# Optimization experiments

Hardware: AMD Instinct MI355X
Metric: run time of the kernel (lower is better)

The kernel has to match this reference:

```python
import jax, jax.numpy as jnp
import numpy as np

B, D, F, E, G = 2048, 1024, 4096, 16, 2
EPS = 1e-9
LN_EPS = 1e-5


def setup_inputs() -> dict:
    key = jax.random.key(0)
    ks = jax.random.split(key, 10)
    s_in = 1.0 / np.sqrt(D)
    s_out = 1.0 / np.sqrt(F)
    return {
        "cycle_curve_data": jax.random.normal(ks[0], (B, D), jnp.float32),
        "logits": jax.random.normal(ks[1], (B, E), jnp.float32),
        "moe_masks": jax.random.randint(ks[2], (B, E), 0, 2, jnp.int32),
        "ew_in": jax.random.uniform(ks[3], (E, D, F), jnp.float32, -s_in, s_in),
        "ew_out": jax.random.uniform(ks[4], (E, F, D), jnp.float32, -s_out, s_out),
        "eb_out": jax.random.uniform(ks[5], (E, D), jnp.float32, -s_out, s_out),
        "gw_in": jax.random.uniform(ks[6], (G, D, F), jnp.float32, -s_in, s_in),
        "gw_out": jax.random.uniform(ks[7], (G, F, D), jnp.float32, -s_out, s_out),
        "gb_out": jax.random.uniform(ks[8], (G, D), jnp.float32, -s_out, s_out),
        "ln_gamma": jnp.ones((D,), jnp.float32),
        "ln_beta": jnp.zeros((D,), jnp.float32),
    }


def _moe_forward(x, logits, moe_masks, ew_in, ew_out, eb_out, gw_in, gw_out, gb_out, ln_gamma, ln_beta):
    b = x.shape[0]
    mask = (moe_masks == 1).astype(logits.dtype)          # [B,E]
    raw = jax.nn.softmax(logits, axis=1)                   # [B,E]
    gates = raw * mask
    gates = gates / (jnp.sum(gates, axis=1, keepdims=True) + EPS)
    # Per-expert MLPBlockGELU over all tokens; gate=0 zeroes out non-dispatched
    # tokens exactly as MOEDispatcher.combine does.
    h = jax.nn.gelu(jnp.einsum('bd,edf->ebf', x, ew_in), approximate=False)  # [E,B,F]
    eout = jnp.einsum('ebf,efd->ebd', h, ew_out) + eb_out[:, None, :]        # [E,B,D]
    moe_out = jnp.einsum('be,ebd->bd', gates, eout).astype(jnp.bfloat16)     # combine + bf16 cast
    # general experts (dense, added to routed output; bf16+f32 promotes to f32)
    gh = jax.nn.gelu(jnp.einsum('bd,gdf->gbf', x, gw_in), approximate=False)
    gout = jnp.einsum('gbf,gfd->gbd', gh, gw_out) + gb_out[:, None, :]       # [G,B,D]
    final = jnp.sum(gout, axis=0) + moe_out                                  # f32
    # residual + LayerNorm
    y = final + x
    mu = jnp.mean(y, axis=-1, keepdims=True)
    var = jnp.mean(jnp.square(y - mu), axis=-1, keepdims=True)
    final_out = (y - mu) * jax.lax.rsqrt(var + LN_EPS) * ln_gamma + ln_beta
    # training losses
    expert_logits = jnp.mean(raw, axis=0)                                    # [E]
    expert_sample_count = jnp.sum((gates != 0).astype(raw.dtype), axis=0) / b
    aug_loss = jnp.mean(expert_logits * expert_sample_count)
    s = jnp.sum(raw * mask) / b
    guide_loss = (1.0 - s) * (1.0 - s)
    return final_out, aug_loss, guide_loss


def reference(cycle_curve_data, logits, moe_masks, ew_in, ew_out, eb_out, gw_in, gw_out, gb_out, ln_gamma, ln_beta):
    return _moe_forward(cycle_curve_data, logits, moe_masks, ew_in, ew_out, eb_out,
                        gw_in, gw_out, gb_out, ln_gamma, ln_beta)
```

## Files before the change

### kernel.cpp

```cpp
#include <hip/hip_runtime.h>
#include <hip/hip_bf16.h>

#define B_TOK 2048
#define DDIM 1024
#define FDIM 4096
#define NE 16
#define NG 2
#define BD ((long)B_TOK * DDIM)

typedef unsigned short u16;
typedef __attribute__((ext_vector_type(8))) short bf16x8;
typedef __attribute__((ext_vector_type(4))) float f32x4;

__device__ inline u16 f2bf(float x) {
  union { float f; unsigned u; } v; v.f = x;
  return (u16)((v.u + 0x7fffu + ((v.u >> 16) & 1u)) >> 16);
}
__device__ inline float bfround(float x) {
  union { float f; unsigned u; } v; v.f = x;
  v.u = ((v.u + 0x7fffu + ((v.u >> 16) & 1u)) >> 16) << 16;
  return v.f;
}
__device__ inline float fast_erf(float x) {
  float ax = fabsf(x);
  float t = __builtin_amdgcn_rcpf(1.0f + 0.3275911f * ax);
  float poly = t * (0.254829592f + t * (-0.284496736f + t * (1.421413741f +
               t * (-1.453152027f + t * 1.061405429f))));
  float r = 1.0f - poly * __expf(-ax * ax);
  return copysignf(r, x);
}
__device__ inline float gelu_exact(float x) {
  return 0.5f * x * (1.0f + fast_erf(x * 0.70710678118654752440f));
}
__device__ inline void gload16(const void* g, void* l) {
  __builtin_amdgcn_global_load_lds((const __attribute__((address_space(1))) void*)g,
                                   (__attribute__((address_space(3))) void*)l, 16, 0, 0);
}
__device__ inline float waveSum(float v) {
  v += __shfl_down(v, 32); v += __shfl_down(v, 16); v += __shfl_down(v, 8);
  v += __shfl_down(v, 4);  v += __shfl_down(v, 2);  v += __shfl_down(v, 1);
  return v;
}

__global__ __launch_bounds__(256) void gating_kernel(
    const float* __restrict__ logits, const int* __restrict__ masks,
    float* __restrict__ gates, float* __restrict__ loss)
{
  const int b = blockIdx.x * 256 + threadIdx.x;
  const int lane = threadIdx.x & 63;
  const float* lr = logits + (long)b * NE;
  const int*   mr = masks  + (long)b * NE;
  float raw[NE]; int mk[NE];
  float mx = -1e30f;
#pragma unroll
  for (int e = 0; e < NE; ++e) { raw[e] = lr[e]; mx = fmaxf(mx, raw[e]); }
  float s = 0.f;
#pragma unroll
  for (int e = 0; e < NE; ++e) { raw[e] = expf(raw[e] - mx); s += raw[e]; }
  float inv = 1.0f / s;
#pragma unroll
  for (int e = 0; e < NE; ++e) raw[e] *= inv;
  float gs = 0.f;
#pragma unroll
  for (int e = 0; e < NE; ++e) { mk[e] = (mr[e] == 1); gs += mk[e] ? raw[e] : 0.f; }
  float ginv = 1.0f / (gs + 1e-9f);
  float* gr = gates + (long)b * NE;
#pragma unroll
  for (int e = 0; e < NE; ++e) gr[e] = (mk[e] ? raw[e] : 0.f) * ginv;
#pragma unroll
  for (int e = 0; e < NE; ++e) {
    float cs = waveSum(raw[e]);
    float cc = waveSum(mk[e] ? 1.f : 0.f);
    if (lane == 0) { atomicAdd(&loss[e], cs); atomicAdd(&loss[NE + e], cc); }
  }
  float t = waveSum(gs);
  if (lane == 0) atomicAdd(&loss[32], t);
}

__global__ void finalize_loss(const float* __restrict__ loss, float* __restrict__ out2) {
  if (threadIdx.x == 0) {
    float aug = 0.f;
    for (int e = 0; e < NE; ++e)
      aug += (loss[e] / (float)B_TOK) * (loss[NE + e] / (float)B_TOK);
    aug *= (1.0f / NE);
    float s = loss[32] / (float)B_TOK;
    out2[0] = aug;
    out2[1] = (1.f - s) * (1.f - s);
  }
}

__global__ __launch_bounds__(256) void compact_kernel(
    const int* __restrict__ masks, int* __restrict__ tok,
    int* __restrict__ pos, int* __restrict__ cnts)
{
  const int e = blockIdx.x, tid = threadIdx.x;
  const int lane = tid & 63, wave = tid >> 6;
  __shared__ int wcnt[4];
  __shared__ int runbase;
  if (tid == 0) runbase = 0;
  __syncthreads();
  for (int b0 = 0; b0 < B_TOK; b0 += 256) {
    int b = b0 + tid;
    int m = (masks[(long)b * NE + e] == 1);
    unsigned long long bal = __ballot(m);
    int pre = __popcll(bal & ((1ull << lane) - 1ull));
    if (lane == 0) wcnt[wave] = __popcll(bal);
    __syncthreads();
    int base = runbase;
    for (int w = 0; w < wave; ++w) base += wcnt[w];
    if (m) {
      int p = base + pre;
      tok[(e << 11) + p] = b;
      pos[(long)b * NE + e] = p;
    } else {
      pos[(long)b * NE + e] = -1;
    }
    __syncthreads();
    if (tid == 0) runbase += wcnt[0] + wcnt[1] + wcnt[2] + wcnt[3];
    __syncthreads();
  }
  const int cnt = runbase;
  const int cnt_pad = (cnt + 127) & ~127;
  for (int i = cnt + tid; i < cnt_pad; i += 256)
    tok[(e << 11) + i] = 0;
  if (tid == 0) { cnts[e] = cnt; cnts[NE + e] = cnt_pad; }
}

__global__ __launch_bounds__(256) void cvt_x_kernel(const float* __restrict__ x, u16* __restrict__ xb) {
  long i = ((long)blockIdx.x * 256 + threadIdx.x) * 4;
  float4 v = *(const float4*)&x[i];
  ushort4 o; o.x = f2bf(v.x); o.y = f2bf(v.y); o.z = f2bf(v.z); o.w = f2bf(v.w);
  *(ushort4*)&xb[i] = o;
}

__global__ __launch_bounds__(256) void bias_init_kernel(
    const float* __restrict__ gates, const float* __restrict__ eb,
    float* __restrict__ moe_bias)
{
  long i = (long)blockIdx.x * 256 + threadIdx.x;
  int b = (int)(i >> 10), d = (int)(i & 1023);
  const float* gr = gates + (long)b * NE;
  float s = 0.f;
#pragma unroll
  for (int e = 0; e < NE; ++e) s += gr[e] * eb[e * DDIM + d];
  moe_bias[i] = s;
}

__global__ __launch_bounds__(256) void transpose_cvt(
    const float* __restrict__ src, u16* __restrict__ dst,
    int R, int C, long sZ, long dZ)
{
  __shared__ float t[64][65];
  const float* s = src + (long)blockIdx.z * sZ;
  u16* d = dst + (long)blockIdx.z * dZ;
  const int c0 = blockIdx.x * 64, r0 = blockIdx.y * 64;
  const int tid = threadIdx.x;
#pragma unroll
  for (int it = 0; it < 4; ++it) {
    int idx = tid + it * 256;
    int r = idx >> 4, cq = (idx & 15) * 4;
    float4 v = *(const float4*)&s[(long)(r0 + r) * C + c0 + cq];
    t[r][cq] = v.x; t[r][cq + 1] = v.y; t[r][cq + 2] = v.z; t[r][cq + 3] = v.w;
  }
  __syncthreads();
#pragma unroll
  for (int it = 0; it < 4; ++it) {
    int idx = tid + it * 256;
    int c = idx >> 4, rq = (idx & 15) * 4;
    ushort4 o;
    o.x = f2bf(t[rq][c]); o.y = f2bf(t[rq+1][c]); o.z = f2bf(t[rq+2][c]); o.w = f2bf(t[rq+3][c]);
    *(ushort4*)&d[(long)(c0 + c) * R + r0 + rq] = o;
  }
}

template<int MODE>
__global__ __launch_bounds__(256) void gemm128(
    const u16* __restrict__ A, int lda, long aZ,
    const u16* __restrict__ Bm, int ldb, long bZ,
    int klen,
    u16* __restrict__ H, long hZ,
    float* __restrict__ C, long cZ,
    const int* __restrict__ tok, const int* __restrict__ cnts, int ebase)
{
  int lin = ((int)blockIdx.z * gridDim.y + blockIdx.y) * gridDim.x + blockIdx.x;
  const int T = gridDim.x * gridDim.y * gridDim.z;
  lin = (lin & 7) * (T >> 3) + (lin >> 3);
  const int bx = lin % gridDim.x;
  const int rest = lin / gridDim.x;
  const int by = rest % gridDim.y;
  const int bz = rest / gridDim.y;

  const int zi = (MODE == 2) ? (bz >> 2) : bz;
  const int ks = (MODE == 2) ? (bz & 3) * klen : 0;
  const int m0 = by * 128, n0 = bx * 128;
  if (MODE != 2 && cnts && m0 >= cnts[NE + ebase + zi]) return;

  __shared__ u16 sA[3][128 * 32];
  __shared__ u16 sB[3][128 * 32];
  const u16* Az = A + (long)zi * aZ;
  const u16* Bz = Bm + (long)zi * bZ;
  const int tid = threadIdx.x, lane = tid & 63, wave = tid >> 6;

  const int off = tid * 16;
  const int sr  = off >> 6;
  const int ske = (off & 63) >> 1;
  int arow0 = m0 + sr, arow1 = m0 + sr + 64;
  if (MODE == 0 && tok) {
    const int* tz = tok + ((ebase + zi) << 11);
    arow0 = tz[arow0]; arow1 = tz[arow1];
  }
  const u16* gA0 = Az + (long)arow0 * lda + ks + ske;
  const u16* gA1 = Az + (long)arow1 * lda + ks + ske;
  const u16* gB0 = Bz + (long)(n0 + sr) * ldb + ks + ske;
  const u16* gB1 = gB0 + (long)64 * ldb;

  const int wr = wave >> 1, wc = wave & 1;
  const int fr = lane & 15, fk = (lane >> 4) * 8;
  const int rAo = (wr * 64 + fr) * 32 + fk;
  const int rBo = (wc * 64 + fr) * 32 + fk;

  f32x4 zero = {0.f, 0.f, 0.f, 0.f};
  f32x4 acc[4][4];
#pragma unroll
  for (int m = 0; m < 4; ++m)
#pragma unroll
    for (int n = 0; n < 4; ++n) acc[m][n] = zero;

  auto STAGE = [&](u16* dA, u16* dB, int t) {
    const int kk = t << 5;
    gload16(gA0 + kk, dA + wave * 512);
    gload16(gA1 + kk, dA + 2048 + wave * 512);
    gload16(gB0 + kk, dB + wave * 512);
    gload16(gB1 + kk, dB + 2048 + wave * 512);
  };
  auto COMPUTE = [&](const u16* bA, const u16* bB) {
    bf16x8 av[4], bv[4];
#pragma unroll
    for (int m = 0; m < 4; ++m) av[m] = *(const bf16x8*)(bA + rAo + m * 512);
#pragma unroll
    for (int n = 0; n < 4; ++n) bv[n] = *(const bf16x8*)(bB + rBo + n * 512);
#pragma unroll
    for (int m = 0; m < 4; ++m)
#pragma unroll
      for (int n = 0; n < 4; ++n)
        acc[m][n] = __builtin_amdgcn_mfma_f32_16x16x32_bf16(av[m], bv[n], acc[m][n], 0, 0, 0);
  };

#define PIPE(SA, SB, KIDX, CA, CB)                                   \
  STAGE(SA, SB, KIDX);                                               \
  asm volatile("s_waitcnt vmcnt(8)" ::: "memory");                   \
  __builtin_amdgcn_s_barrier();                                      \
  asm volatile("" ::: "memory");                                     \
  COMPUTE(CA, CB);                                                   \
  asm volatile("" ::: "memory");                                     \
  __builtin_amdgcn_s_barrier();                                      \
  asm volatile("" ::: "memory");

  const int nt = klen >> 5;
  STAGE(sA[0], sB[0], 0);
  STAGE(sA[1], sB[1], 1);
  for (int t = 0; t + 2 < nt; t += 3) {
    PIPE(sA[2], sB[2], t + 2, sA[0], sB[0]);
    PIPE(sA[0], sB[0], t + 3, sA[1], sB[1]);
    PIPE(sA[1], sB[1], t + 4, sA[2], sB[2]);
  }
  asm volatile("s_waitcnt vmcnt(4)" ::: "memory");
  __builtin_amdgcn_s_barrier();
  asm volatile("" ::: "memory");
  COMPUTE(sA[0], sB[0]);
  asm volatile("s_waitcnt vmcnt(0)" ::: "memory");
  __builtin_amdgcn_s_barrier();
  asm volatile("" ::: "memory");
  COMPUTE(sA[1], sB[1]);
#undef PIPE

  const int er = m0 + wr * 64 + (lane >> 4) * 4;
  const int ec = n0 + wc * 64 + fr;
  if (MODE == 0) {
    u16* Hz = H + (long)zi * hZ;
#pragma unroll
    for (int m = 0; m < 4; ++m)
#pragma unroll
      for (int n = 0; n < 4; ++n) {
        f32x4 v = acc[m][n];
        int rb = er + m * 16, cb = ec + n * 16;
#pragma unroll
        for (int j = 0; j < 4; ++j)
          Hz[(long)(rb + j) * FDIM + cb] = f2bf(gelu_exact(v[j]));
      }
  } else if (MODE == 1) {
    float* Cz = C + (long)(ebase + zi) * cZ;
#pragma unroll
    for (int m = 0; m < 4; ++m)
#pragma unroll
      for (int n = 0; n < 4; ++n) {
        f32x4 v = acc[m][n];
        int rb = er + m * 16, cb = ec + n * 16;
#pragma unroll
        for (int j = 0; j < 4; ++j)
          Cz[(long)(rb + j) * DDIM + cb] = v[j];
      }
  } else {
    float* Cz = C + (long)bz * cZ;
#pragma unroll
    for (int m = 0; m < 4; ++m)
#pragma unroll
      for (int n = 0; n < 4; ++n) {
        f32x4 v = acc[m][n];
        int rb = er + m * 16, cb = ec + n * 16;
#pragma unroll
        for (int j = 0; j < 4; ++j)
          Cz[(long)(rb + j) * DDIM + cb] = v[j];
      }
  }
}

__global__ __launch_bounds__(256) void combine_ln_kernel(
    const float* __restrict__ x, const float* __restrict__ moe_bias,
    const float* __restrict__ Eout, const float* __restrict__ gen_p,
    const float* __restrict__ gb,
    const int* __restrict__ pos, const float* __restrict__ gates,
    const float* __restrict__ gamma, const float* __restrict__ beta,
    float* __restrict__ out)
{
  const int b = blockIdx.x, tid = threadIdx.x;
  const int lane = tid & 63, wave = tid >> 6;
  const long base = (long)b * DDIM;
  __shared__ int posr[NE];
  __shared__ float gr[NE];
  __shared__ float red[4];
  if (tid < NE) { posr[tid] = pos[(long)b * NE + tid]; gr[tid] = gates[(long)b * NE + tid]; }
  __syncthreads();
  float y[4];
  float ls = 0.f;
#pragma unroll
  for (int i = 0; i < 4; ++i) {
    int d = tid + i * 256;
    long idx = base + d;
    float moe = moe_bias[idx];
#pragma unroll
    for (int e = 0; e < NE; ++e) {
      int p = posr[e];
      if (p >= 0) moe += gr[e] * Eout[((long)e * B_TOK + p) * DDIM + d];
    }
    moe = bfround(moe);
    float ge = gb[d] + gb[DDIM + d];
#pragma unroll
    for (int sl = 0; sl < 8; ++sl) ge += gen_p[(long)sl * BD + idx];
    y[i] = moe + ge + x[idx];
    ls += y[i];
  }
  float t = waveSum(ls);
  if (lane == 0) red[wave] = t;
  __syncthreads();
  float mean = (red[0] + red[1] + red[2] + red[3]) * (1.0f / DDIM);
  __syncthreads();
  float vs = 0.f;
#pragma unroll
  for (int i = 0; i < 4; ++i) { float d2 = y[i] - mean; vs += d2 * d2; }
  t = waveSum(vs);
  if (lane == 0) red[wave] = t;
  __syncthreads();
  float var = (red[0] + red[1] + red[2] + red[3]) * (1.0f / DDIM);
  float inv = rsqrtf(var + 1e-5f);
#pragma unroll
  for (int i = 0; i < 4; ++i) {
    int d = tid + i * 256;
    out[base + d] = (y[i] - mean) * inv * gamma[d] + beta[d];
  }
}

extern "C" void kernel_launch(void* const* d_in, const int* in_sizes, int n_in,
                              void* d_out, int out_size, void* d_ws, size_t ws_size,
                              hipStream_t stream)
{
  const float* x      = (const float*)d_in[0];
  const float* logits = (const float*)d_in[1];
  const int*   masks  = (const int*)d_in[2];
  const float* ew_in  = (const float*)d_in[3];
  const float* ew_out = (const float*)d_in[4];
  const float* eb_out = (const float*)d_in[5];
  const float* gw_in  = (const float*)d_in[6];
  const float* gw_out = (const float*)d_in[7];
  const float* gb_out = (const float*)d_in[8];
  const float* gamma  = (const float*)d_in[9];
  const float* beta   = (const float*)d_in[10];
  float* out = (float*)d_out;

  char* w = (char*)d_ws;
  size_t off = 0;
  auto alloc = [&](size_t bytes) -> void* {
    off = (off + 4095) & ~(size_t)4095;
    void* p = w + off; off += bytes; return p;
  };
  const long DF = (long)DDIM * FDIM;
  const long BF = (long)B_TOK * FDIM;

  float* gates    = (float*)alloc((size_t)B_TOK * NE * 4);
  float* loss     = (float*)alloc(64 * 4);
  int*   tok      = (int*)alloc((size_t)NE * B_TOK * 4);
  int*   pos      = (int*)alloc((size_t)B_TOK * NE * 4);
  int*   cnts     = (int*)alloc(2 * NE * 4);
  u16*   xb       = (u16*)alloc((size_t)BD * 2);
  float* moe_bias = (float*)alloc((size_t)BD * 4);
  float* gen_p    = (float*)alloc(8 * (size_t)BD * 4);
  float* Eout     = (float*)alloc((size_t)NE * BD * 4);
  u16*   WgInT    = (u16*)alloc((size_t)NG * DF * 2);
  u16*   WgOutT   = (u16*)alloc((size_t)NG * DF * 2);
  u16*   Hg       = (u16*)alloc((size_t)NG * BF * 2);

  const size_t per = 2 * (size_t)DF * 2 + (size_t)BF * 2 + 3 * 4096;
  int CE = 16;
  while (CE > 1 && off + (size_t)CE * per > ws_size) CE >>= 1;
  u16* WinT  = (u16*)alloc((size_t)CE * DF * 2);
  u16* WoutT = (u16*)alloc((size_t)CE * DF * 2);
  u16* Hb    = (u16*)alloc((size_t)CE * BF * 2);

  hipMemsetAsync(loss, 0, 64 * 4, stream);
  gating_kernel<<<8, 256, 0, stream>>>(logits, masks, gates, loss);
  finalize_loss<<<1, 64, 0, stream>>>(loss, out + BD);
  compact_kernel<<<NE, 256, 0, stream>>>(masks, tok, pos, cnts);
  cvt_x_kernel<<<2048, 256, 0, stream>>>(x, xb);
  bias_init_kernel<<<8192, 256, 0, stream>>>(gates, eb_out, moe_bias);

  for (int e0 = 0; e0 < NE; e0 += CE) {
    transpose_cvt<<<dim3(FDIM/64, DDIM/64, CE), 256, 0, stream>>>(
        ew_in + (long)e0 * DF, WinT, DDIM, FDIM, DF, DF);
    transpose_cvt<<<dim3(DDIM/64, FDIM/64, CE), 256, 0, stream>>>(
        ew_out + (long)e0 * DF, WoutT, FDIM, DDIM, DF, DF);
    gemm128<0><<<dim3(FDIM/128, B_TOK/128, CE), 256, 0, stream>>>(
        xb, DDIM, 0L, WinT, DDIM, DF, DDIM,
        Hb, BF, nullptr, 0L, tok, cnts, e0);
    gemm128<1><<<dim3(DDIM/128, B_TOK/128, CE), 256, 0, stream>>>(
        Hb, FDIM, BF, WoutT, FDIM, DF, FDIM,
        nullptr, 0L, Eout, BD, nullptr, cnts, e0);
  }

  transpose_cvt<<<dim3(FDIM/64, DDIM/64, NG), 256, 0, stream>>>(
      gw_in, WgInT, DDIM, FDIM, DF, DF);
  transpose_cvt<<<dim3(DDIM/64, FDIM/64, NG), 256, 0, stream>>>(
      gw_out, WgOutT, FDIM, DDIM, DF, DF);
  gemm128<0><<<dim3(FDIM/128, B_TOK/128, NG), 256, 0, stream>>>(
      xb, DDIM, 0L, WgInT, DDIM, DF, DDIM,
      Hg, BF, nullptr, 0L, nullptr, nullptr, 0);
  gemm128<2><<<dim3(DDIM/128, B_TOK/128, NG * 4), 256, 0, stream>>>(
      Hg, FDIM, BF, WgOutT, FDIM, DF, FDIM / 4,
      nullptr, 0L, gen_p, BD, nullptr, nullptr, 0);

  combine_ln_kernel<<<B_TOK, 256, 0, stream>>>(
      x, moe_bias, Eout, gen_p, gb_out, pos, gates, gamma, beta, out);
}
```

Baseline: 774.2 us.

## Replace 128x128 GEMMs with 256-row 512-thread tiles, merging experts and general branches

Swaps the 128x128 tile GEMM for a 256-row tile kernel with 8 waves, a 64-wide K step and XOR-swizzled LDS, using a single-stage pipeline for the up projection and a double-stage one for the down projection. The routed and general experts now run in one launch per projection (z up to 18) instead of a per-chunk loop plus separate general launches. The split-K for the general down projection is dropped, so combine reads only two partials. Expert token counts are padded to 256. The larger tiles aim for more data reuse and fewer launches, but cost more LDS and registers, give lower occupancy and waste more work on padded rows.

```diff
diff --git a/kernel.cpp b/kernel.cpp
--- a/kernel.cpp
+++ b/kernel.cpp
@@ -120,7 +120,7 @@
     __syncthreads();
   }
   const int cnt = runbase;
-  const int cnt_pad = (cnt + 127) & ~127;
+  const int cnt_pad = (cnt + 255) & ~255;
   for (int i = cnt + tid; i < cnt_pad; i += 256)
     tok[(e << 11) + i] = 0;
   if (tid == 0) { cnts[e] = cnt; cnts[NE + e] = cnt_pad; }
@@ -173,141 +173,139 @@
   }
 }
 
-template<int MODE>
-__global__ __launch_bounds__(256) void gemm128(
+template<int PROJ>
+__global__ __launch_bounds__(512, 2) void gemm256(
     const u16* __restrict__ A, int lda, long aZ,
-    const u16* __restrict__ Bm, int ldb, long bZ,
+    const u16* __restrict__ Bm, int ldb,
     int klen,
-    u16* __restrict__ H, long hZ,
-    float* __restrict__ C, long cZ,
-    const int* __restrict__ tok, const int* __restrict__ cnts, int ebase)
-{
-  int lin = ((int)blockIdx.z * gridDim.y + blockIdx.y) * gridDim.x + blockIdx.x;
+    u16* __restrict__ H,
+    float* __restrict__ Eout, float* __restrict__ genp,
+    const int* __restrict__ tok, const int* __restrict__ cnts)
+{
+  constexpr int BN    = PROJ ? 128 : 256;
+  constexpr int NBS   = BN / 64;
+  constexpr int DEPTH = PROJ ? 2 : 1;
+  constexpr int NBUF  = DEPTH + 1;
+  constexpr int WN    = BN / 64;
+  constexpr int MI    = PROJ ? 4 : 8;
+  __shared__ u16 lds[NBUF][16384 + BN * 64];
+
+  int lin = ((int)blockIdx.z * gridDim.x + blockIdx.x) * gridDim.y + blockIdx.y;
   const int T = gridDim.x * gridDim.y * gridDim.z;
   lin = (lin & 7) * (T >> 3) + (lin >> 3);
-  const int bx = lin % gridDim.x;
-  const int rest = lin / gridDim.x;
-  const int by = rest % gridDim.y;
-  const int bz = rest / gridDim.y;
-
-  const int zi = (MODE == 2) ? (bz >> 2) : bz;
-  const int ks = (MODE == 2) ? (bz & 3) * klen : 0;
-  const int m0 = by * 128, n0 = bx * 128;
-  if (MODE != 2 && cnts && m0 >= cnts[NE + ebase + zi]) return;
-
-  __shared__ u16 sA[3][128 * 32];
-  __shared__ u16 sB[3][128 * 32];
-  const u16* Az = A + (long)zi * aZ;
-  const u16* Bz = Bm + (long)zi * bZ;
+  const int by = lin % gridDim.y;  int tmp = lin / gridDim.y;
+  const int bx = tmp % gridDim.x;  const int z = tmp / gridDim.x;
+
+  const int m0 = by * 256, n0 = bx * BN;
+  if (z < NE && m0 >= cnts[NE + z]) return;
+
   const int tid = threadIdx.x, lane = tid & 63, wave = tid >> 6;
-
-  const int off = tid * 16;
-  const int sr  = off >> 6;
-  const int ske = (off & 63) >> 1;
-  int arow0 = m0 + sr, arow1 = m0 + sr + 64;
-  if (MODE == 0 && tok) {
-    const int* tz = tok + ((ebase + zi) << 11);
-    arow0 = tz[arow0]; arow1 = tz[arow1];
-  }
-  const u16* gA0 = Az + (long)arow0 * lda + ks + ske;
-  const u16* gA1 = Az + (long)arow1 * lda + ks + ske;
-  const u16* gB0 = Bz + (long)(n0 + sr) * ldb + ks + ske;
-  const u16* gB1 = gB0 + (long)64 * ldb;
-
-  const int wr = wave >> 1, wc = wave & 1;
-  const int fr = lane & 15, fk = (lane >> 4) * 8;
-  const int rAo = (wr * 64 + fr) * 32 + fk;
-  const int rBo = (wc * 64 + fr) * 32 + fk;
+  const int wr = wave / WN, wc = wave % WN;
+  const int srow = wave * 8 + (lane >> 3);
+  const int swz  = ((lane & 7) * 8) ^ ((lane >> 3) * 8);
+
+  const u16* aSrc[4];
+  const u16* bSrc[NBS];
+  const u16* Bz = Bm + (long)z * ((long)DDIM * FDIM);
+#pragma unroll
+  for (int s = 0; s < 4; ++s) {
+    int r = m0 + s * 64 + srow;
+    if (PROJ == 0 && z < NE) r = tok[(z << 11) + r];
+    const u16* Abase = (PROJ == 0) ? A : A + (long)z * aZ;
+    aSrc[s] = Abase + (long)r * lda + swz;
+  }
+#pragma unroll
+  for (int s = 0; s < NBS; ++s)
+    bSrc[s] = Bz + (long)(n0 + s * 64 + srow) * ldb + swz;
+
+  auto STAGE = [&](int buf, int kk) {
+    u16* la = &lds[buf][0];
+    u16* lb = &lds[buf][16384];
+#pragma unroll
+    for (int s = 0; s < 4; ++s)
+      gload16(aSrc[s] + kk, la + s * 4096 + wave * 512);
+#pragma unroll
+    for (int s = 0; s < NBS; ++s)
+      gload16(bSrc[s] + kk, lb + s * 4096 + wave * 512);
+  };
 
   f32x4 zero = {0.f, 0.f, 0.f, 0.f};
-  f32x4 acc[4][4];
-#pragma unroll
-  for (int m = 0; m < 4; ++m)
-#pragma unroll
-    for (int n = 0; n < 4; ++n) acc[m][n] = zero;
-
-  auto STAGE = [&](u16* dA, u16* dB, int t) {
-    const int kk = t << 5;
-    gload16(gA0 + kk, dA + wave * 512);
-    gload16(gA1 + kk, dA + 2048 + wave * 512);
-    gload16(gB0 + kk, dB + wave * 512);
-    gload16(gB1 + kk, dB + 2048 + wave * 512);
+  f32x4 acc[MI][4];
+#pragma unroll
+  for (int mi = 0; mi < MI; ++mi)
+#pragma unroll
+    for (int ni = 0; ni < 4; ++ni) acc[mi][ni] = zero;
+
+  auto COMPUTE = [&](int buf) {
+    const u16* la = &lds[buf][0];
+    const u16* lb = &lds[buf][16384];
+#pragma unroll
+    for (int k2 = 0; k2 < 2; ++k2) {
+      const int fk = (lane >> 4) * 8 + k2 * 32;
+      bf16x8 bv[4];
+#pragma unroll
+      for (int ni = 0; ni < 4; ++ni) {
+        int br = wc * 64 + ni * 16 + (lane & 15);
+        bv[ni] = *(const bf16x8*)(lb + br * 64 + (fk ^ ((br & 7) << 3)));
+      }
+#pragma unroll
+      for (int mi = 0; mi < MI; ++mi) {
+        int ar = wr * (MI * 16) + mi * 16 + (lane & 15);
+        bf16x8 av = *(const bf16x8*)(la + ar * 64 + (fk ^ ((ar & 7) << 3)));
+#pragma unroll
+        for (int ni = 0; ni < 4; ++ni)
+          acc[mi][ni] = __builtin_amdgcn_mfma_f32_16x16x32_bf16(av, bv[ni], acc[mi][ni], 0, 0, 0);
+      }
+    }
   };
-  auto COMPUTE = [&](const u16* bA, const u16* bB) {
-    bf16x8 av[4], bv[4];
-#pragma unroll
-    for (int m = 0; m < 4; ++m) av[m] = *(const bf16x8*)(bA + rAo + m * 512);
-#pragma unroll
-    for (int n = 0; n < 4; ++n) bv[n] = *(const bf16x8*)(bB + rBo + n * 512);
-#pragma unroll
-    for (int m = 0; m < 4; ++m)
-#pragma unroll
-      for (int n = 0; n < 4; ++n)
-        acc[m][n] = __builtin_amdgcn_mfma_f32_16x16x32_bf16(av[m], bv[n], acc[m][n], 0, 0, 0);
-  };
-
-#define PIPE(SA, SB, KIDX, CA, CB)                                   \
-  STAGE(SA, SB, KIDX);                                               \
-  asm volatile("s_waitcnt vmcnt(8)" ::: "memory");                   \
-  __builtin_amdgcn_s_barrier();                                      \
-  asm volatile("" ::: "memory");                                     \
-  COMPUTE(CA, CB);                                                   \
-  asm volatile("" ::: "memory");                                     \
-  __builtin_amdgcn_s_barrier();                                      \
-  asm volatile("" ::: "memory");
-
-  const int nt = klen >> 5;
-  STAGE(sA[0], sB[0], 0);
-  STAGE(sA[1], sB[1], 1);
-  for (int t = 0; t + 2 < nt; t += 3) {
-    PIPE(sA[2], sB[2], t + 2, sA[0], sB[0]);
-    PIPE(sA[0], sB[0], t + 3, sA[1], sB[1]);
-    PIPE(sA[1], sB[1], t + 4, sA[2], sB[2]);
-  }
-  asm volatile("s_waitcnt vmcnt(4)" ::: "memory");
-  __builtin_amdgcn_s_barrier();
-  asm volatile("" ::: "memory");
-  COMPUTE(sA[0], sB[0]);
-  asm volatile("s_waitcnt vmcnt(0)" ::: "memory");
-  __builtin_amdgcn_s_barrier();
-  asm volatile("" ::: "memory");
-  COMPUTE(sA[1], sB[1]);
-#undef PIPE
-
-  const int er = m0 + wr * 64 + (lane >> 4) * 4;
-  const int ec = n0 + wc * 64 + fr;
-  if (MODE == 0) {
-    u16* Hz = H + (long)zi * hZ;
-#pragma unroll
-    for (int m = 0; m < 4; ++m)
-#pragma unroll
-      for (int n = 0; n < 4; ++n) {
-        f32x4 v = acc[m][n];
-        int rb = er + m * 16, cb = ec + n * 16;
+
+  const int NT = klen >> 6;
+  STAGE(0, 0);
+  if (DEPTH == 2) STAGE(1, 64);
+  int cur = 0, stg = DEPTH;
+  for (int t = 0; t < NT; ++t) {
+    const int ahead = t + DEPTH;
+    if (ahead < NT) {
+      STAGE(stg, ahead << 6);
+      if (PROJ) asm volatile("s_waitcnt vmcnt(12)" ::: "memory");
+      else      asm volatile("s_waitcnt vmcnt(8)"  ::: "memory");
+    } else if (PROJ == 1 && t + 1 < NT) {
+      asm volatile("s_waitcnt vmcnt(6)" ::: "memory");
+    } else {
+      asm volatile("s_waitcnt vmcnt(0)" ::: "memory");
+    }
+    __builtin_amdgcn_s_barrier();
+    asm volatile("" ::: "memory");
+    COMPUTE(cur);
+    asm volatile("" ::: "memory");
+    __builtin_amdgcn_s_barrier();
+    asm volatile("" ::: "memory");
+    cur = (cur + 1 == NBUF) ? 0 : cur + 1;
+    stg = (stg + 1 == NBUF) ? 0 : stg + 1;
+  }
+
+  const int er = m0 + wr * (MI * 16) + (lane >> 4) * 4;
+  const int ec = n0 + wc * 64 + (lane & 15);
+  if (PROJ == 0) {
+    u16* Hz = H + (long)z * ((long)B_TOK * FDIM);
+#pragma unroll
+    for (int mi = 0; mi < MI; ++mi)
+#pragma unroll
+      for (int ni = 0; ni < 4; ++ni) {
+        f32x4 v = acc[mi][ni];
+        int rb = er + mi * 16, cb = ec + ni * 16;
 #pragma unroll
         for (int j = 0; j < 4; ++j)
           Hz[(long)(rb + j) * FDIM + cb] = f2bf(gelu_exact(v[j]));
       }
-  } else if (MODE == 1) {
-    float* Cz = C + (long)(ebase + zi) * cZ;
-#pragma unroll
-    for (int m = 0; m < 4; ++m)
-#pragma unroll
-      for (int n = 0; n < 4; ++n) {
-        f32x4 v = acc[m][n];
-        int rb = er + m * 16, cb = ec + n * 16;
-#pragma unroll
-        for (int j = 0; j < 4; ++j)
-          Cz[(long)(rb + j) * DDIM + cb] = v[j];
-      }
   } else {
-    float* Cz = C + (long)bz * cZ;
-#pragma unroll
-    for (int m = 0; m < 4; ++m)
-#pragma unroll
-      for (int n = 0; n < 4; ++n) {
-        f32x4 v = acc[m][n];
-        int rb = er + m * 16, cb = ec + n * 16;
+    float* Cz = (z < NE) ? (Eout + (long)z * BD) : (genp + (long)(z - NE) * BD);
+#pragma unroll
+    for (int mi = 0; mi < MI; ++mi)
+#pragma unroll
+      for (int ni = 0; ni < 4; ++ni) {
+        f32x4 v = acc[mi][ni];
+        int rb = er + mi * 16, cb = ec + ni * 16;
 #pragma unroll
         for (int j = 0; j < 4; ++j)
           Cz[(long)(rb + j) * DDIM + cb] = v[j];
@@ -344,9 +342,7 @@
       if (p >= 0) moe += gr[e] * Eout[((long)e * B_TOK + p) * DDIM + d];
     }
     moe = bfround(moe);
-    float ge = gb[d] + gb[DDIM + d];
-#pragma unroll
-    for (int sl = 0; sl < 8; ++sl) ge += gen_p[(long)sl * BD + idx];
+    float ge = gb[d] + gb[DDIM + d] + gen_p[idx] + gen_p[BD + idx];
     y[i] = moe + ge + x[idx];
     ls += y[i];
   }
@@ -395,6 +391,7 @@
   };
   const long DF = (long)DDIM * FDIM;
   const long BF = (long)B_TOK * FDIM;
+  const int  NZ = NE + NG;
 
   float* gates    = (float*)alloc((size_t)B_TOK * NE * 4);
   float* loss     = (float*)alloc(64 * 4);
@@ -403,18 +400,11 @@
   int*   cnts     = (int*)alloc(2 * NE * 4);
   u16*   xb       = (u16*)alloc((size_t)BD * 2);
   float* moe_bias = (float*)alloc((size_t)BD * 4);
-  float* gen_p    = (float*)alloc(8 * (size_t)BD * 4);
+  float* gen_p    = (float*)alloc((size_t)NG * BD * 4);
   float* Eout     = (float*)alloc((size_t)NE * BD * 4);
-  u16*   WgInT    = (u16*)alloc((size_t)NG * DF * 2);
-  u16*   WgOutT   = (u16*)alloc((size_t)NG * DF * 2);
-  u16*   Hg       = (u16*)alloc((size_t)NG * BF * 2);
-
-  const size_t per = 2 * (size_t)DF * 2 + (size_t)BF * 2 + 3 * 4096;
-  int CE = 16;
-  while (CE > 1 && off + (size_t)CE * per > ws_size) CE >>= 1;
-  u16* WinT  = (u16*)alloc((size_t)CE * DF * 2);
-  u16* WoutT = (u16*)alloc((size_t)CE * DF * 2);
-  u16* Hb    = (u16*)alloc((size_t)CE * BF * 2);
+  u16*   WinT     = (u16*)alloc((size_t)NZ * DF * 2);
+  u16*   WoutT    = (u16*)alloc((size_t)NZ * DF * 2);
+  u16*   Hb       = (u16*)alloc((size_t)NZ * BF * 2);
 
   hipMemsetAsync(loss, 0, 64 * 4, stream);
   gating_kernel<<<8, 256, 0, stream>>>(logits, masks, gates, loss);
@@ -423,29 +413,21 @@
   cvt_x_kernel<<<2048, 256, 0, stream>>>(x, xb);
   bias_init_kernel<<<8192, 256, 0, stream>>>(gates, eb_out, moe_bias);
 
-  for (int e0 = 0; e0 < NE; e0 += CE) {
-    transpose_cvt<<<dim3(FDIM/64, DDIM/64, CE), 256, 0, stream>>>(
-        ew_in + (long)e0 * DF, WinT, DDIM, FDIM, DF, DF);
-    transpose_cvt<<<dim3(DDIM/64, FDIM/64, CE), 256, 0, stream>>>(
-        ew_out + (long)e0 * DF, WoutT, FDIM, DDIM, DF, DF);
-    gemm128<0><<<dim3(FDIM/128, B_TOK/128, CE), 256, 0, stream>>>(
-        xb, DDIM, 0L, WinT, DDIM, DF, DDIM,
-        Hb, BF, nullptr, 0L, tok, cnts, e0);
-    gemm128<1><<<dim3(DDIM/128, B_TOK/128, CE), 256, 0, stream>>>(
-        Hb, FDIM, BF, WoutT, FDIM, DF, FDIM,
-        nullptr, 0L, Eout, BD, nullptr, cnts, e0);
-  }
-
+  transpose_cvt<<<dim3(FDIM/64, DDIM/64, NE), 256, 0, stream>>>(
+      ew_in, WinT, DDIM, FDIM, DF, DF);
   transpose_cvt<<<dim3(FDIM/64, DDIM/64, NG), 256, 0, stream>>>(
-      gw_in, WgInT, DDIM, FDIM, DF, DF);
+      gw_in, WinT + (long)NE * DF, DDIM, FDIM, DF, DF);
+  transpose_cvt<<<dim3(DDIM/64, FDIM/64, NE), 256, 0, stream>>>(
+      ew_out, WoutT, FDIM, DDIM, DF, DF);
   transpose_cvt<<<dim3(DDIM/64, FDIM/64, NG), 256, 0, stream>>>(
-      gw_out, WgOutT, FDIM, DDIM, DF, DF);
-  gemm128<0><<<dim3(FDIM/128, B_TOK/128, NG), 256, 0, stream>>>(
-      xb, DDIM, 0L, WgInT, DDIM, DF, DDIM,
-      Hg, BF, nullptr, 0L, nullptr, nullptr, 0);
-  gemm128<2><<<dim3(DDIM/128, B_TOK/128, NG * 4), 256, 0, stream>>>(
-      Hg, FDIM, BF, WgOutT, FDIM, DF, FDIM / 4,
-      nullptr, 0L, gen_p, BD, nullptr, nullptr, 0);
+      gw_out, WoutT + (long)NE * DF, FDIM, DDIM, DF, DF);
+
+  gemm256<0><<<dim3(FDIM/256, B_TOK/256, NZ), 512, 0, stream>>>(
+      xb, DDIM, 0L, WinT, DDIM, DDIM,
+      Hb, nullptr, nullptr, tok, cnts);
+  gemm256<1><<<dim3(DDIM/128, B_TOK/256, NZ), 512, 0, stream>>>(
+      Hb, FDIM, BF, WoutT, FDIM, FDIM,
+      nullptr, Eout, gen_p, nullptr, cnts);
 
   combine_ln_kernel<<<B_TOK, 256, 0, stream>>>(
       x, moe_bias, Eout, gen_p, gb_out, pos, gates, gamma, beta, out);
```

Measured after the change: 923.6 us. 1.19x slower.

## Merge expert and general GEMMs into single launches with swizzled LDS layout

Applied to the files above, without the earlier changes.

Routed and general experts now go through one pair of batched GEMM launches over all 18 weight sets, replacing the chunked per-expert loop and the separate general-expert split-K path. The LDS k-offset is XOR-swizzled by row to cut bank conflicts on fragment reads. The first projection's block order is changed so consecutive blocks walk M first, sharing the same weight tile. The workspace now has to hold every expert's transposed weights and hidden activations at once, and the general down-projection loses its split-K parallelism in exchange for one fewer intermediate pass.

```diff
diff --git a/kernel.cpp b/kernel.cpp
--- a/kernel.cpp
+++ b/kernel.cpp
@@ -173,51 +173,53 @@
   }
 }
 
-template<int MODE>
-__global__ __launch_bounds__(256) void gemm128(
+template<int PROJ>
+__global__ __launch_bounds__(256) void gemm128s(
     const u16* __restrict__ A, int lda, long aZ,
-    const u16* __restrict__ Bm, int ldb, long bZ,
-    int klen,
-    u16* __restrict__ H, long hZ,
-    float* __restrict__ C, long cZ,
-    const int* __restrict__ tok, const int* __restrict__ cnts, int ebase)
-{
-  int lin = ((int)blockIdx.z * gridDim.y + blockIdx.y) * gridDim.x + blockIdx.x;
+    const u16* __restrict__ Bm, int ldb,
+    u16* __restrict__ H,
+    float* __restrict__ Eout, float* __restrict__ genp,
+    const int* __restrict__ tok, const int* __restrict__ cnts)
+{
+  constexpr int KLEN = PROJ ? FDIM : DDIM;
+  int lin;
+  if (PROJ == 0)
+    lin = ((int)blockIdx.z * gridDim.x + blockIdx.x) * gridDim.y + blockIdx.y;
+  else
+    lin = ((int)blockIdx.z * gridDim.y + blockIdx.y) * gridDim.x + blockIdx.x;
   const int T = gridDim.x * gridDim.y * gridDim.z;
   lin = (lin & 7) * (T >> 3) + (lin >> 3);
-  const int bx = lin % gridDim.x;
-  const int rest = lin / gridDim.x;
-  const int by = rest % gridDim.y;
-  const int bz = rest / gridDim.y;
-
-  const int zi = (MODE == 2) ? (bz >> 2) : bz;
-  const int ks = (MODE == 2) ? (bz & 3) * klen : 0;
+  int bx, by, z;
+  if (PROJ == 0) { by = lin % gridDim.y; int r2 = lin / gridDim.y; bx = r2 % gridDim.x; z = r2 / gridDim.x; }
+  else           { bx = lin % gridDim.x; int r2 = lin / gridDim.x; by = r2 % gridDim.y; z = r2 / gridDim.y; }
+
   const int m0 = by * 128, n0 = bx * 128;
-  if (MODE != 2 && cnts && m0 >= cnts[NE + ebase + zi]) return;
+  if (z < NE && m0 >= cnts[NE + z]) return;
 
   __shared__ u16 sA[3][128 * 32];
   __shared__ u16 sB[3][128 * 32];
-  const u16* Az = A + (long)zi * aZ;
-  const u16* Bz = Bm + (long)zi * bZ;
+  const u16* Az = (PROJ == 0) ? A : A + (long)z * aZ;
+  const u16* Bz = Bm + (long)z * ((long)DDIM * FDIM);
   const int tid = threadIdx.x, lane = tid & 63, wave = tid >> 6;
 
   const int off = tid * 16;
   const int sr  = off >> 6;
-  const int ske = (off & 63) >> 1;
+  const int ske = ((off & 63) >> 1) ^ (((sr >> 1) & 3) << 3);
   int arow0 = m0 + sr, arow1 = m0 + sr + 64;
-  if (MODE == 0 && tok) {
-    const int* tz = tok + ((ebase + zi) << 11);
+  if (PROJ == 0 && z < NE) {
+    const int* tz = tok + (z << 11);
     arow0 = tz[arow0]; arow1 = tz[arow1];
   }
-  const u16* gA0 = Az + (long)arow0 * lda + ks + ske;
-  const u16* gA1 = Az + (long)arow1 * lda + ks + ske;
-  const u16* gB0 = Bz + (long)(n0 + sr) * ldb + ks + ske;
-  const u16* gB1 = gB0 + (long)64 * ldb;
+  const u16* gA0 = Az + (long)arow0 * lda + ske;
+  const u16* gA1 = Az + (long)arow1 * lda + ske;
+  const u16* gB0 = Bz + (long)(n0 + sr) * ldb + ske;
+  const u16* gB1 = Bz + (long)(n0 + sr + 64) * ldb + ske;
 
   const int wr = wave >> 1, wc = wave & 1;
-  const int fr = lane & 15, fk = (lane >> 4) * 8;
-  const int rAo = (wr * 64 + fr) * 32 + fk;
-  const int rBo = (wc * 64 + fr) * 32 + fk;
+  const int fr = lane & 15;
+  const int fks = ((lane >> 4) * 8) ^ (((fr >> 1) & 3) << 3);
+  const int rAo = (wr * 64 + fr) * 32 + fks;
+  const int rBo = (wc * 64 + fr) * 32 + fks;
 
   f32x4 zero = {0.f, 0.f, 0.f, 0.f};
   f32x4 acc[4][4];
@@ -256,7 +258,7 @@
   __builtin_amdgcn_s_barrier();                                      \
   asm volatile("" ::: "memory");
 
-  const int nt = klen >> 5;
+  const int nt = KLEN >> 5;
   STAGE(sA[0], sB[0], 0);
   STAGE(sA[1], sB[1], 1);
   for (int t = 0; t + 2 < nt; t += 3) {
@@ -276,8 +278,8 @@
 
   const int er = m0 + wr * 64 + (lane >> 4) * 4;
   const int ec = n0 + wc * 64 + fr;
-  if (MODE == 0) {
-    u16* Hz = H + (long)zi * hZ;
+  if (PROJ == 0) {
+    u16* Hz = H + (long)z * ((long)B_TOK * FDIM);
 #pragma unroll
     for (int m = 0; m < 4; ++m)
 #pragma unroll
@@ -288,20 +290,8 @@
         for (int j = 0; j < 4; ++j)
           Hz[(long)(rb + j) * FDIM + cb] = f2bf(gelu_exact(v[j]));
       }
-  } else if (MODE == 1) {
-    float* Cz = C + (long)(ebase + zi) * cZ;
-#pragma unroll
-    for (int m = 0; m < 4; ++m)
-#pragma unroll
-      for (int n = 0; n < 4; ++n) {
-        f32x4 v = acc[m][n];
-        int rb = er + m * 16, cb = ec + n * 16;
-#pragma unroll
-        for (int j = 0; j < 4; ++j)
-          Cz[(long)(rb + j) * DDIM + cb] = v[j];
-      }
   } else {
-    float* Cz = C + (long)bz * cZ;
+    float* Cz = (z < NE) ? (Eout + (long)z * BD) : (genp + (long)(z - NE) * BD);
 #pragma unroll
     for (int m = 0; m < 4; ++m)
 #pragma unroll
@@ -344,9 +334,7 @@
       if (p >= 0) moe += gr[e] * Eout[((long)e * B_TOK + p) * DDIM + d];
     }
     moe = bfround(moe);
-    float ge = gb[d] + gb[DDIM + d];
-#pragma unroll
-    for (int sl = 0; sl < 8; ++sl) ge += gen_p[(long)sl * BD + idx];
+    float ge = gb[d] + gb[DDIM + d] + gen_p[idx] + gen_p[BD + idx];
     y[i] = moe + ge + x[idx];
     ls += y[i];
   }
@@ -395,6 +383,7 @@
   };
   const long DF = (long)DDIM * FDIM;
   const long BF = (long)B_TOK * FDIM;
+  const int  NZ = NE + NG;
 
   float* gates    = (float*)alloc((size_t)B_TOK * NE * 4);
   float* loss     = (float*)alloc(64 * 4);
@@ -403,18 +392,11 @@
   int*   cnts     = (int*)alloc(2 * NE * 4);
   u16*   xb       = (u16*)alloc((size_t)BD * 2);
   float* moe_bias = (float*)alloc((size_t)BD * 4);
-  float* gen_p    = (float*)alloc(8 * (size_t)BD * 4);
+  float* gen_p    = (float*)alloc((size_t)NG * BD * 4);
   float* Eout     = (float*)alloc((size_t)NE * BD * 4);
-  u16*   WgInT    = (u16*)alloc((size_t)NG * DF * 2);
-  u16*   WgOutT   = (u16*)alloc((size_t)NG * DF * 2);
-  u16*   Hg       = (u16*)alloc((size_t)NG * BF * 2);
-
-  const size_t per = 2 * (size_t)DF * 2 + (size_t)BF * 2 + 3 * 4096;
-  int CE = 16;
-  while (CE > 1 && off + (size_t)CE * per > ws_size) CE >>= 1;
-  u16* WinT  = (u16*)alloc((size_t)CE * DF * 2);
-  u16* WoutT = (u16*)alloc((size_t)CE * DF * 2);
-  u16* Hb    = (u16*)alloc((size_t)CE * BF * 2);
+  u16*   WinT     = (u16*)alloc((size_t)NZ * DF * 2);
+  u16*   WoutT    = (u16*)alloc((size_t)NZ * DF * 2);
+  u16*   Hb       = (u16*)alloc((size_t)NZ * BF * 2);
 
   hipMemsetAsync(loss, 0, 64 * 4, stream);
   gating_kernel<<<8, 256, 0, stream>>>(logits, masks, gates, loss);
@@ -423,29 +405,21 @@
   cvt_x_kernel<<<2048, 256, 0, stream>>>(x, xb);
   bias_init_kernel<<<8192, 256, 0, stream>>>(gates, eb_out, moe_bias);
 
-  for (int e0 = 0; e0 < NE; e0 += CE) {
-    transpose_cvt<<<dim3(FDIM/64, DDIM/64, CE), 256, 0, stream>>>(
-        ew_in + (long)e0 * DF, WinT, DDIM, FDIM, DF, DF);
-    transpose_cvt<<<dim3(DDIM/64, FDIM/64, CE), 256, 0, stream>>>(
-        ew_out + (long)e0 * DF, WoutT, FDIM, DDIM, DF, DF);
-    gemm128<0><<<dim3(FDIM/128, B_TOK/128, CE), 256, 0, stream>>>(
-        xb, DDIM, 0L, WinT, DDIM, DF, DDIM,
-        Hb, BF, nullptr, 0L, tok, cnts, e0);
-    gemm128<1><<<dim3(DDIM/128, B_TOK/128, CE), 256, 0, stream>>>(
-        Hb, FDIM, BF, WoutT, FDIM, DF, FDIM,
-        nullptr, 0L, Eout, BD, nullptr, cnts, e0);
-  }
-
+  transpose_cvt<<<dim3(FDIM/64, DDIM/64, NE), 256, 0, stream>>>(
+      ew_in, WinT, DDIM, FDIM, DF, DF);
   transpose_cvt<<<dim3(FDIM/64, DDIM/64, NG), 256, 0, stream>>>(
-      gw_in, WgInT, DDIM, FDIM, DF, DF);
+      gw_in, WinT + (long)NE * DF, DDIM, FDIM, DF, DF);
+  transpose_cvt<<<dim3(DDIM/64, FDIM/64, NE), 256, 0, stream>>>(
+      ew_out, WoutT, FDIM, DDIM, DF, DF);
   transpose_cvt<<<dim3(DDIM/64, FDIM/64, NG), 256, 0, stream>>>(
-      gw_out, WgOutT, FDIM, DDIM, DF, DF);
-  gemm128<0><<<dim3(FDIM/128, B_TOK/128, NG), 256, 0, stream>>>(
-      xb, DDIM, 0L, WgInT, DDIM, DF, DDIM,
-      Hg, BF, nullptr, 0L, nullptr, nullptr, 0);
-  gemm128<2><<<dim3(DDIM/128, B_TOK/128, NG * 4), 256, 0, stream>>>(
-      Hg, FDIM, BF, WgOutT, FDIM, DF, FDIM / 4,
-      nullptr, 0L, gen_p, BD, nullptr, nullptr, 0);
+      gw_out, WoutT + (long)NE * DF, FDIM, DDIM, DF, DF);
+
+  gemm128s<0><<<dim3(FDIM/128, B_TOK/128, NZ), 256, 0, stream>>>(
+      xb, DDIM, 0L, WinT, DDIM,
+      Hb, nullptr, nullptr, tok, cnts);
+  gemm128s<1><<<dim3(DDIM/128, B_TOK/128, NZ), 256, 0, stream>>>(
+      Hb, FDIM, BF, WoutT, FDIM,
+      nullptr, Eout, gen_p, nullptr, cnts);
 
   combine_ln_kernel<<<B_TOK, 256, 0, stream>>>(
       x, moe_bias, Eout, gen_p, gb_out, pos, gates, gamma, beta, out);
```

After: 1.097 ms. +41.8%, slower.
